# Performance work log

Measured on AMD Instinct MI355X. Metric: run time of the kernel, lower is better.

Reference implementation:

```python
import jax, jax.numpy as jnp
import numpy as np

N = 1_048_576      # flattened batch (forward reshapes to (-1, 4))
Q_DIM = 4
HIDDEN = 64
DC = Q_DIM // 2    # q_dim_changed = 2
NUM_LO = (DC * DC - DC) // 2  # = 1
SLOPE = 0.01       # torch leaky_relu default negative slope


def setup_inputs() -> dict:
    key = jax.random.key(0)
    ks = jax.random.split(key, 9)
    def lin(kw, kb, fan_out, fan_in):
        bound = 1.0 / np.sqrt(fan_in)
        W = jax.random.uniform(kw, (fan_out, fan_in), jnp.float32, -bound, bound)
        b = jax.random.uniform(kb, (fan_out,), jnp.float32, -bound, bound)
        return W, b
    x = jax.random.normal(ks[0], (N, Q_DIM), jnp.float32)
    W1, b1 = lin(ks[1], ks[2], HIDDEN, Q_DIM)
    W2, b2 = lin(ks[3], ks[4], HIDDEN, HIDDEN)
    W_Ld, b_Ld = lin(ks[5], ks[6], DC, HIDDEN)
    W_Lo, b_Lo = lin(ks[7], ks[8], NUM_LO, HIDDEN)
    return {"x": x, "W1": W1, "b1": b1, "W2": W2, "b2": b2,
            "W_Ld": W_Ld, "b_Ld": b_Ld, "W_Lo": W_Lo, "b_Lo": b_Lo}


def reference(x, W1, b1, W2, b2, W_Ld, b_Ld, W_Lo, b_Lo):
    q = x.reshape(-1, Q_DIM)                      # (n, 4)
    n = q.shape[0]
    h1 = jax.nn.leaky_relu(q @ W1.T + b1, SLOPE)  # (n, 64)
    h2 = jax.nn.leaky_relu(h1 @ W2.T + b2, SLOPE) # (n, 64); dropout is eval-mode identity
    Ld = jax.nn.softplus(h2 @ W_Ld.T + b_Ld)      # (n, 2) positive diagonal
    Lo = h2 @ W_Lo.T + b_Lo                       # (n, 1) strictly-lower entries
    rows, cols = jnp.tril_indices(DC, -1)         # strictly lower triangle, row-major
    diag = jnp.arange(DC)
    L = jnp.zeros((n, DC, DC), dtype=q.dtype)
    L = L.at[:, rows, cols].set(Lo)               # scatter Lo (matches torch boolean-mask fill order)
    L = L.at[:, diag, diag].set(Ld)               # diag_embed(Ld)
    H = jnp.einsum('nij,nkj->nik', L, L) + 1e-9 * jnp.eye(DC, dtype=q.dtype)
    return H
```

## Files before the change

kernel.cpp:

```cpp
#include <hip/hip_runtime.h>


typedef __attribute__((ext_vector_type(8))) short bf16x8;
typedef __attribute__((ext_vector_type(4))) float f32x4;
typedef __attribute__((ext_vector_type(2))) float f32x2;

#define BLOCK_THREADS  256
#define ROWS_PER_GROUP 256

__device__ __forceinline__ float lrelu(float a) {
    return fmaxf(a, 0.01f * a);
}

__device__ __forceinline__ f32x2 lrelu2(f32x2 a) {
    return __builtin_elementwise_max(a, a * 0.01f);
}

__device__ __forceinline__ float softplus(float v) {
    return fmaxf(v, 0.0f) + log1pf(expf(-fabsf(v)));
}

__device__ __forceinline__ unsigned cvt_pk_bf16(float lo, float hi) {
    unsigned r;
    asm("v_cvt_pk_bf16_f32 %0, %1, %2" : "=v"(r) : "v"(lo), "v"(hi));
    return r;
}

__device__ __forceinline__ float lo_of(float v, unsigned pk, bool hi_half) {
    const float h = __uint_as_float(hi_half ? (pk & 0xFFFF0000u) : (pk << 16));
    return v - h;
}

__global__ __launch_bounds__(BLOCK_THREADS) void dln_mfma(
    const float* __restrict__ x,
    const float* __restrict__ W1,  const float* __restrict__ b1,
    const float* __restrict__ W2,  const float* __restrict__ b2,
    const float* __restrict__ WLd, const float* __restrict__ bLd,
    const float* __restrict__ WLo, const float* __restrict__ bLo,
    float* __restrict__ out)
{
    const int tid  = threadIdx.x;
    const int lane = tid & 63;
    const int wv   = tid >> 6;
    const int quad = lane >> 4;
    const int c    = lane & 15;

    const int wbase = blockIdx.x * ROWS_PER_GROUP + wv * 64;

    float4 xv[4];
#pragma unroll
    for (int it = 0; it < 4; ++it)
        xv[it] = ((const float4*)x)[wbase + it * 16 + c];

    bf16x8 a1[4];
#pragma unroll
    for (int mt = 0; mt < 4; ++mt) {
        const int nu = 32 * (mt >> 1) + 8 * (c >> 2) + 4 * (mt & 1) + (c & 3);
        const float4 w = *(const float4*)(W1 + 4 * nu);
        const float bb = b1[nu];
        const unsigned h01 = cvt_pk_bf16(w.x, w.y);
        const unsigned h23 = cvt_pk_bf16(w.z, w.w);
        uint4 u = make_uint4(0u, 0u, 0u, 0u);
        if (quad == 0) {
            const unsigned t = cvt_pk_bf16(bb, 0.0f);
            const float bl = bb - __uint_as_float(t << 16);
            u.x = h01; u.y = h23;
            u.z = cvt_pk_bf16(bb, bl);
        } else if (quad == 1) {
            u.x = cvt_pk_bf16(lo_of(w.x, h01, false), lo_of(w.y, h01, true));
            u.y = cvt_pk_bf16(lo_of(w.z, h23, false), lo_of(w.w, h23, true));
            u.z = h01; u.w = h23;
        }
        a1[mt] = __builtin_bit_cast(bf16x8, u);
    }

    bf16x8 afrag[4][2];
    f32x4 b2v[4];
#pragma unroll
    for (int mt = 0; mt < 4; ++mt) {
        const int nu = 32 * (mt >> 1) + 8 * (c >> 2) + 4 * (mt & 1) + (c & 3);
        const float* wr = W2 + nu * 64 + 8 * quad;
#pragma unroll
        for (int s = 0; s < 2; ++s) {
            const float4 f0 = *(const float4*)(wr + 32 * s);
            const float4 f1 = *(const float4*)(wr + 32 * s + 4);
            uint4 u;
            u.x = cvt_pk_bf16(f0.x, f0.y);
            u.y = cvt_pk_bf16(f0.z, f0.w);
            u.z = cvt_pk_bf16(f1.x, f1.y);
            u.w = cvt_pk_bf16(f1.z, f1.w);
            afrag[mt][s] = __builtin_bit_cast(bf16x8, u);
        }
        b2v[mt] = *(const f32x4*)(b2 + 32 * (mt >> 1) + 4 * (mt & 1) + 8 * quad);
    }

    bf16x8 hA[2][2];
    {
        const float* hw = (c == 0) ? WLd : (c == 1) ? (WLd + 64) : WLo;
#pragma unroll
        for (int s = 0; s < 2; ++s) {
            uint4 uh = make_uint4(0u, 0u, 0u, 0u);
            uint4 ul = make_uint4(0u, 0u, 0u, 0u);
            if (c < 3) {
                const float* p = hw + 32 * s + 8 * quad;
                const float4 f0 = *(const float4*)(p);
                const float4 f1 = *(const float4*)(p + 4);
                uh.x = cvt_pk_bf16(f0.x, f0.y);
                uh.y = cvt_pk_bf16(f0.z, f0.w);
                uh.z = cvt_pk_bf16(f1.x, f1.y);
                uh.w = cvt_pk_bf16(f1.z, f1.w);
                ul.x = cvt_pk_bf16(lo_of(f0.x, uh.x, false), lo_of(f0.y, uh.x, true));
                ul.y = cvt_pk_bf16(lo_of(f0.z, uh.y, false), lo_of(f0.w, uh.y, true));
                ul.z = cvt_pk_bf16(lo_of(f1.x, uh.z, false), lo_of(f1.y, uh.z, true));
                ul.w = cvt_pk_bf16(lo_of(f1.z, uh.w, false), lo_of(f1.w, uh.w, true));
            }
            hA[s][0] = __builtin_bit_cast(bf16x8, uh);
            hA[s][1] = __builtin_bit_cast(bf16x8, ul);
        }
    }
    const f32x4 hinit = (quad == 0)
        ? (f32x4){bLd[0], bLd[1], bLo[0], 0.0f}
        : (f32x4){0.0f, 0.0f, 0.0f, 0.0f};

#pragma unroll
    for (int it = 0; it < 4; ++it) {
        const unsigned xh01 = cvt_pk_bf16(xv[it].x, xv[it].y);
        const unsigned xh23 = cvt_pk_bf16(xv[it].z, xv[it].w);
        uint4 ub = make_uint4(0u, 0u, 0u, 0u);
        if (quad == 0) {
            ub.x = xh01; ub.y = xh23; ub.z = 0x3F803F80u;
        } else if (quad == 1) {
            ub.x = xh01; ub.y = xh23;
            ub.z = cvt_pk_bf16(lo_of(xv[it].x, xh01, false), lo_of(xv[it].y, xh01, true));
            ub.w = cvt_pk_bf16(lo_of(xv[it].z, xh23, false), lo_of(xv[it].w, xh23, true));
        }
        const bf16x8 bx = __builtin_bit_cast(bf16x8, ub);

        f32x4 acc1[4];
#pragma unroll
        for (int mt = 0; mt < 4; ++mt)
            acc1[mt] = __builtin_amdgcn_mfma_f32_16x16x32_bf16(
                a1[mt], bx, (f32x4){0.0f, 0.0f, 0.0f, 0.0f}, 0, 0, 0);

        uint4 u0, u1;
        {
            const f32x2 p0 = lrelu2((f32x2){acc1[0][0], acc1[0][1]});
            const f32x2 p1 = lrelu2((f32x2){acc1[0][2], acc1[0][3]});
            const f32x2 p2 = lrelu2((f32x2){acc1[1][0], acc1[1][1]});
            const f32x2 p3 = lrelu2((f32x2){acc1[1][2], acc1[1][3]});
            const f32x2 p4 = lrelu2((f32x2){acc1[2][0], acc1[2][1]});
            const f32x2 p5 = lrelu2((f32x2){acc1[2][2], acc1[2][3]});
            const f32x2 p6 = lrelu2((f32x2){acc1[3][0], acc1[3][1]});
            const f32x2 p7 = lrelu2((f32x2){acc1[3][2], acc1[3][3]});
            u0.x = cvt_pk_bf16(p0[0], p0[1]);
            u0.y = cvt_pk_bf16(p1[0], p1[1]);
            u0.z = cvt_pk_bf16(p2[0], p2[1]);
            u0.w = cvt_pk_bf16(p3[0], p3[1]);
            u1.x = cvt_pk_bf16(p4[0], p4[1]);
            u1.y = cvt_pk_bf16(p5[0], p5[1]);
            u1.z = cvt_pk_bf16(p6[0], p6[1]);
            u1.w = cvt_pk_bf16(p7[0], p7[1]);
        }
        const bf16x8 bf0 = __builtin_bit_cast(bf16x8, u0);
        const bf16x8 bf1 = __builtin_bit_cast(bf16x8, u1);

        uint4 v0, v1;
#pragma unroll
        for (int mt = 0; mt < 4; ++mt) {
            f32x4 acc = b2v[mt];
            acc = __builtin_amdgcn_mfma_f32_16x16x32_bf16(afrag[mt][0], bf0, acc, 0, 0, 0);
            acc = __builtin_amdgcn_mfma_f32_16x16x32_bf16(afrag[mt][1], bf1, acc, 0, 0, 0);
            const f32x2 hlo = lrelu2((f32x2){acc[0], acc[1]});
            const f32x2 hhi = lrelu2((f32x2){acc[2], acc[3]});
            const unsigned pa = cvt_pk_bf16(hlo[0], hlo[1]);
            const unsigned pb = cvt_pk_bf16(hhi[0], hhi[1]);
            if (mt == 0)      { v0.x = pa; v0.y = pb; }
            else if (mt == 1) { v0.z = pa; v0.w = pb; }
            else if (mt == 2) { v1.x = pa; v1.y = pb; }
            else              { v1.z = pa; v1.w = pb; }
        }
        const bf16x8 bh0 = __builtin_bit_cast(bf16x8, v0);
        const bf16x8 bh1 = __builtin_bit_cast(bf16x8, v1);

        f32x4 ha = hinit;
        f32x4 hb = (f32x4){0.0f, 0.0f, 0.0f, 0.0f};
        ha = __builtin_amdgcn_mfma_f32_16x16x32_bf16(hA[0][0], bh0, ha, 0, 0, 0);
        hb = __builtin_amdgcn_mfma_f32_16x16x32_bf16(hA[0][1], bh0, hb, 0, 0, 0);
        ha = __builtin_amdgcn_mfma_f32_16x16x32_bf16(hA[1][0], bh1, ha, 0, 0, 0);
        hb = __builtin_amdgcn_mfma_f32_16x16x32_bf16(hA[1][1], bh1, hb, 0, 0, 0);

        if (quad == 0) {
            const float ld0 = softplus(ha[0] + hb[0]);
            const float ld1 = softplus(ha[1] + hb[1]);
            const float lo  = ha[2] + hb[2];
            float4 o;
            o.x = fmaf(ld0, ld0, 1e-9f);
            o.y = ld0 * lo;
            o.z = o.y;
            o.w = fmaf(lo, lo, fmaf(ld1, ld1, 1e-9f));
            reinterpret_cast<float4*>(out)[wbase + it * 16 + c] = o;
        }
    }
}

__global__ __launch_bounds__(256) void dln_tail(
    const float* __restrict__ x,
    const float* __restrict__ W1,  const float* __restrict__ b1,
    const float* __restrict__ W2,  const float* __restrict__ b2,
    const float* __restrict__ WLd, const float* __restrict__ bLd,
    const float* __restrict__ WLo, const float* __restrict__ bLo,
    float* __restrict__ out, int row0, int nrows)
{
    const int row = row0 + blockIdx.x * 256 + threadIdx.x;
    if (row >= nrows) return;
    const float4 qv = reinterpret_cast<const float4*>(x)[row];
    float h1[64];
#pragma unroll
    for (int j = 0; j < 64; ++j) {
        float a = b1[j];
        a = fmaf(qv.x, W1[4 * j + 0], a);
        a = fmaf(qv.y, W1[4 * j + 1], a);
        a = fmaf(qv.z, W1[4 * j + 2], a);
        a = fmaf(qv.w, W1[4 * j + 3], a);
        h1[j] = lrelu(a);
    }
    float ld0 = bLd[0], ld1 = bLd[1], lo = bLo[0];
#pragma unroll 4
    for (int j = 0; j < 64; ++j) {
        float a0 = b2[j], a1 = 0.0f;
        const float* w = W2 + 64 * j;
#pragma unroll
        for (int k = 0; k < 64; k += 2) {
            a0 = fmaf(h1[k],     w[k],     a0);
            a1 = fmaf(h1[k + 1], w[k + 1], a1);
        }
        const float a = lrelu(a0 + a1);
        ld0 = fmaf(a, WLd[j],      ld0);
        ld1 = fmaf(a, WLd[64 + j], ld1);
        lo  = fmaf(a, WLo[j],      lo);
    }
    ld0 = softplus(ld0);
    ld1 = softplus(ld1);
    float4 o;
    o.x = fmaf(ld0, ld0, 1e-9f);
    o.y = ld0 * lo;
    o.z = o.y;
    o.w = fmaf(lo, lo, fmaf(ld1, ld1, 1e-9f));
    reinterpret_cast<float4*>(out)[row] = o;
}

extern "C" void kernel_launch(void* const* d_in, const int* in_sizes, int n_in,
                              void* d_out, int out_size, void* d_ws, size_t ws_size,
                              hipStream_t stream)
{
    const float* x   = (const float*)d_in[0];
    const float* W1  = (const float*)d_in[1];
    const float* b1  = (const float*)d_in[2];
    const float* W2  = (const float*)d_in[3];
    const float* b2  = (const float*)d_in[4];
    const float* WLd = (const float*)d_in[5];
    const float* bLd = (const float*)d_in[6];
    const float* WLo = (const float*)d_in[7];
    const float* bLo = (const float*)d_in[8];
    float* out = (float*)d_out;

    const int nrows   = in_sizes[0] / 4;
    const int ngroups = nrows / ROWS_PER_GROUP;
    const int nfull   = ngroups * ROWS_PER_GROUP;
    const int rem     = nrows - nfull;

    if (ngroups > 0)
        dln_mfma<<<ngroups, BLOCK_THREADS, 0, stream>>>(
            x, W1, b1, W2, b2, WLd, bLd, WLo, bLo, out);
    if (rem > 0)
        dln_tail<<<(rem + 255) / 256, 256, 0, stream>>>(
            x, W1, b1, W2, b2, WLd, bLd, WLo, bLo, out, nfull, nrows);
}
```

Baseline: 147.5 us.

## Share weight-fragment preparation across waves via LDS instead of per-wave registers

Each wave previously loaded and converted all W1, W2 and head weight fragments into registers on its own. Now the four waves split that setup work, write the bf16 fragments to shared memory, synchronize once, and read them back from LDS inside the row loop. A launch-bounds hint of four blocks per CU is also added to cap register use and raise occupancy. In exchange, the main loop issues LDS reads per iteration and the block pays one barrier.

```diff
diff --git a/kernel.cpp b/kernel.cpp
--- a/kernel.cpp
+++ b/kernel.cpp
@@ -31,7 +31,7 @@
     return v - h;
 }
 
-__global__ __launch_bounds__(BLOCK_THREADS) void dln_mfma(
+__global__ __launch_bounds__(BLOCK_THREADS, 4) void dln_mfma(
     const float* __restrict__ x,
     const float* __restrict__ W1,  const float* __restrict__ b1,
     const float* __restrict__ W2,  const float* __restrict__ b2,
@@ -39,6 +39,11 @@
     const float* __restrict__ WLo, const float* __restrict__ bLo,
     float* __restrict__ out)
 {
+    __shared__ __align__(16) uint4  a1L[4][64];
+    __shared__ __align__(16) uint4  afL[4][2][64];
+    __shared__ __align__(16) float4 b2L[4][64];
+    __shared__ __align__(16) uint4  hAL[2][2][64];
+
     const int tid  = threadIdx.x;
     const int lane = tid & 63;
     const int wv   = tid >> 6;
@@ -52,50 +57,48 @@
     for (int it = 0; it < 4; ++it)
         xv[it] = ((const float4*)x)[wbase + it * 16 + c];
 
-    bf16x8 a1[4];
-#pragma unroll
-    for (int mt = 0; mt < 4; ++mt) {
-        const int nu = 32 * (mt >> 1) + 8 * (c >> 2) + 4 * (mt & 1) + (c & 3);
-        const float4 w = *(const float4*)(W1 + 4 * nu);
-        const float bb = b1[nu];
-        const unsigned h01 = cvt_pk_bf16(w.x, w.y);
-        const unsigned h23 = cvt_pk_bf16(w.z, w.w);
-        uint4 u = make_uint4(0u, 0u, 0u, 0u);
-        if (quad == 0) {
-            const unsigned t = cvt_pk_bf16(bb, 0.0f);
-            const float bl = bb - __uint_as_float(t << 16);
-            u.x = h01; u.y = h23;
-            u.z = cvt_pk_bf16(bb, bl);
-        } else if (quad == 1) {
-            u.x = cvt_pk_bf16(lo_of(w.x, h01, false), lo_of(w.y, h01, true));
-            u.y = cvt_pk_bf16(lo_of(w.z, h23, false), lo_of(w.w, h23, true));
-            u.z = h01; u.w = h23;
-        }
-        a1[mt] = __builtin_bit_cast(bf16x8, u);
-    }
-
-    bf16x8 afrag[4][2];
-    f32x4 b2v[4];
-#pragma unroll
-    for (int mt = 0; mt < 4; ++mt) {
-        const int nu = 32 * (mt >> 1) + 8 * (c >> 2) + 4 * (mt & 1) + (c & 3);
-        const float* wr = W2 + nu * 64 + 8 * quad;
-#pragma unroll
-        for (int s = 0; s < 2; ++s) {
-            const float4 f0 = *(const float4*)(wr + 32 * s);
-            const float4 f1 = *(const float4*)(wr + 32 * s + 4);
-            uint4 u;
-            u.x = cvt_pk_bf16(f0.x, f0.y);
-            u.y = cvt_pk_bf16(f0.z, f0.w);
-            u.z = cvt_pk_bf16(f1.x, f1.y);
-            u.w = cvt_pk_bf16(f1.z, f1.w);
-            afrag[mt][s] = __builtin_bit_cast(bf16x8, u);
-        }
-        b2v[mt] = *(const f32x4*)(b2 + 32 * (mt >> 1) + 4 * (mt & 1) + 8 * quad);
-    }
-
-    bf16x8 hA[2][2];
-    {
+    if (wv == 0) {
+#pragma unroll
+        for (int mt = 0; mt < 4; ++mt) {
+            const int nu = 32 * (mt >> 1) + 8 * (c >> 2) + 4 * (mt & 1) + (c & 3);
+            const float4 w = *(const float4*)(W1 + 4 * nu);
+            const float bb = b1[nu];
+            const unsigned h01 = cvt_pk_bf16(w.x, w.y);
+            const unsigned h23 = cvt_pk_bf16(w.z, w.w);
+            uint4 u = make_uint4(0u, 0u, 0u, 0u);
+            if (quad == 0) {
+                const unsigned t = cvt_pk_bf16(bb, 0.0f);
+                const float bl = bb - __uint_as_float(t << 16);
+                u.x = h01; u.y = h23;
+                u.z = cvt_pk_bf16(bb, bl);
+            } else if (quad == 1) {
+                u.x = cvt_pk_bf16(lo_of(w.x, h01, false), lo_of(w.y, h01, true));
+                u.y = cvt_pk_bf16(lo_of(w.z, h23, false), lo_of(w.w, h23, true));
+                u.z = h01; u.w = h23;
+            }
+            a1L[mt][lane] = u;
+            b2L[mt][lane] = *(const float4*)(b2 + 32 * (mt >> 1) + 4 * (mt & 1) + 8 * quad);
+        }
+    } else if (wv == 1 || wv == 2) {
+        const int mt0 = (wv == 1) ? 0 : 2;
+#pragma unroll
+        for (int k = 0; k < 2; ++k) {
+            const int mt = mt0 + k;
+            const int nu = 32 * (mt >> 1) + 8 * (c >> 2) + 4 * (mt & 1) + (c & 3);
+            const float* wr = W2 + nu * 64 + 8 * quad;
+#pragma unroll
+            for (int s = 0; s < 2; ++s) {
+                const float4 f0 = *(const float4*)(wr + 32 * s);
+                const float4 f1 = *(const float4*)(wr + 32 * s + 4);
+                uint4 u;
+                u.x = cvt_pk_bf16(f0.x, f0.y);
+                u.y = cvt_pk_bf16(f0.z, f0.w);
+                u.z = cvt_pk_bf16(f1.x, f1.y);
+                u.w = cvt_pk_bf16(f1.z, f1.w);
+                afL[mt][s][lane] = u;
+            }
+        }
+    } else {
         const float* hw = (c == 0) ? WLd : (c == 1) ? (WLd + 64) : WLo;
 #pragma unroll
         for (int s = 0; s < 2; ++s) {
@@ -114,10 +117,12 @@
                 ul.z = cvt_pk_bf16(lo_of(f1.x, uh.z, false), lo_of(f1.y, uh.z, true));
                 ul.w = cvt_pk_bf16(lo_of(f1.z, uh.w, false), lo_of(f1.w, uh.w, true));
             }
-            hA[s][0] = __builtin_bit_cast(bf16x8, uh);
-            hA[s][1] = __builtin_bit_cast(bf16x8, ul);
-        }
-    }
+            hAL[s][0][lane] = uh;
+            hAL[s][1][lane] = ul;
+        }
+    }
+    __syncthreads();
+
     const f32x4 hinit = (quad == 0)
         ? (f32x4){bLd[0], bLd[1], bLo[0], 0.0f}
         : (f32x4){0.0f, 0.0f, 0.0f, 0.0f};
@@ -138,9 +143,11 @@
 
         f32x4 acc1[4];
 #pragma unroll
-        for (int mt = 0; mt < 4; ++mt)
+        for (int mt = 0; mt < 4; ++mt) {
+            const bf16x8 a1f = __builtin_bit_cast(bf16x8, a1L[mt][lane]);
             acc1[mt] = __builtin_amdgcn_mfma_f32_16x16x32_bf16(
-                a1[mt], bx, (f32x4){0.0f, 0.0f, 0.0f, 0.0f}, 0, 0, 0);
+                a1f, bx, (f32x4){0.0f, 0.0f, 0.0f, 0.0f}, 0, 0, 0);
+        }
 
         uint4 u0, u1;
         {
@@ -167,9 +174,12 @@
         uint4 v0, v1;
 #pragma unroll
         for (int mt = 0; mt < 4; ++mt) {
-            f32x4 acc = b2v[mt];
-            acc = __builtin_amdgcn_mfma_f32_16x16x32_bf16(afrag[mt][0], bf0, acc, 0, 0, 0);
-            acc = __builtin_amdgcn_mfma_f32_16x16x32_bf16(afrag[mt][1], bf1, acc, 0, 0, 0);
+            const float4 bb = b2L[mt][lane];
+            f32x4 acc = (f32x4){bb.x, bb.y, bb.z, bb.w};
+            const bf16x8 af0 = __builtin_bit_cast(bf16x8, afL[mt][0][lane]);
+            const bf16x8 af1 = __builtin_bit_cast(bf16x8, afL[mt][1][lane]);
+            acc = __builtin_amdgcn_mfma_f32_16x16x32_bf16(af0, bf0, acc, 0, 0, 0);
+            acc = __builtin_amdgcn_mfma_f32_16x16x32_bf16(af1, bf1, acc, 0, 0, 0);
             const f32x2 hlo = lrelu2((f32x2){acc[0], acc[1]});
             const f32x2 hhi = lrelu2((f32x2){acc[2], acc[3]});
             const unsigned pa = cvt_pk_bf16(hlo[0], hlo[1]);
@@ -184,10 +194,16 @@
 
         f32x4 ha = hinit;
         f32x4 hb = (f32x4){0.0f, 0.0f, 0.0f, 0.0f};
-        ha = __builtin_amdgcn_mfma_f32_16x16x32_bf16(hA[0][0], bh0, ha, 0, 0, 0);
-        hb = __builtin_amdgcn_mfma_f32_16x16x32_bf16(hA[0][1], bh0, hb, 0, 0, 0);
-        ha = __builtin_amdgcn_mfma_f32_16x16x32_bf16(hA[1][0], bh1, ha, 0, 0, 0);
-        hb = __builtin_amdgcn_mfma_f32_16x16x32_bf16(hA[1][1], bh1, hb, 0, 0, 0);
+        {
+            const bf16x8 h00 = __builtin_bit_cast(bf16x8, hAL[0][0][lane]);
+            const bf16x8 h01 = __builtin_bit_cast(bf16x8, hAL[0][1][lane]);
+            const bf16x8 h10 = __builtin_bit_cast(bf16x8, hAL[1][0][lane]);
+            const bf16x8 h11 = __builtin_bit_cast(bf16x8, hAL[1][1][lane]);
+            ha = __builtin_amdgcn_mfma_f32_16x16x32_bf16(h00, bh0, ha, 0, 0, 0);
+            hb = __builtin_amdgcn_mfma_f32_16x16x32_bf16(h01, bh0, hb, 0, 0, 0);
+            ha = __builtin_amdgcn_mfma_f32_16x16x32_bf16(h10, bh1, ha, 0, 0, 0);
+            hb = __builtin_amdgcn_mfma_f32_16x16x32_bf16(h11, bh1, hb, 0, 0, 0);
+        }
 
         if (quad == 0) {
             const float ld0 = softplus(ha[0] + hb[0]);
```

After: 131.0 us. -11.2%, faster.
